# Kernel optimization log

Measured on AMD Instinct MI355X. Metric: run time of the kernel, lower is better.

Reference implementation:

```python
import jax, jax.numpy as jnp
import numpy as np

DILATIONS = (1, 2, 4, 8, 16, 32, 64, 128, 256, 512)
K = 3            # kernel_size
CH = 128         # channels
B, T = 4, 16384
L = len(DILATIONS)


def _conv1x1(x, w, b=None):
    # x: [B, Cin, T], w: [Cout, Cin, 1] -> [B, Cout, T]
    y = jnp.einsum('oc,bct->bot', w[..., 0], x)
    return y if b is None else y + b[None, :, None]


def _causal_dilated_conv(x, w, b, d):
    # buffer of zeros of size (K-1)*d concatenated on the left == causal left pad
    pad = (K - 1) * d
    y = jax.lax.conv_general_dilated(
        x, w, window_strides=(1,), padding=[(pad, 0)], rhs_dilation=(d,),
        dimension_numbers=('NCH', 'OIH', 'NCH'))
    return y + b[None, :, None]


def setup_inputs() -> dict:
    key = jax.random.key(0)
    ks = jax.random.split(key, 12)
    s = 0.1  # keep gated activations out of saturation
    return {
        'x': jax.random.normal(ks[0], (B, 1, T), jnp.float32),
        'c': jax.random.normal(ks[1], (B, 1, T), jnp.float32),
        'head_init': jnp.zeros((B, CH, T), jnp.float32),
        'w_re': jax.random.normal(ks[2], (CH, 1, 1), jnp.float32) * s,
        'conv_w': jax.random.normal(ks[3], (L, 2 * CH, CH, K), jnp.float32) * s,
        'conv_b': jax.random.normal(ks[4], (L, 2 * CH), jnp.float32) * s,
        'mix_w': jax.random.normal(ks[5], (L, 2 * CH, 1, 1), jnp.float32) * s,
        'w1x1': jax.random.normal(ks[6], (L, CH, CH, 1), jnp.float32) * s,
        'b1x1': jax.random.normal(ks[7], (L, CH), jnp.float32) * s,
        'w_head': jax.random.normal(ks[8], (1, CH, 1), jnp.float32) * s,
        'b_head': jax.random.normal(ks[9], (1,), jnp.float32) * s,
    }


def reference(x, c, head_init, w_re, conv_w, conv_b, mix_w, w1x1, b1x1, w_head, b_head):
    h = _conv1x1(x, w_re)               # rechannel: [B, CH, T]
    head = head_init                    # head accumulator (zeros == head_input=None)
    for li, d in enumerate(DILATIONS):  # fixed small layer loop (structurally distinct dilations)
        z = _causal_dilated_conv(h, conv_w[li], conv_b[li], d)   # [B, 2CH, T]
        z = z + _conv1x1(c, mix_w[li])                           # conditioning mixer
        post = jnp.tanh(z[:, :CH]) * jax.nn.sigmoid(z[:, CH:])   # gated activation
        h = h + _conv1x1(post, w1x1[li], b1x1[li])               # residual
        head = head + post
    out = _conv1x1(head, w_head, b_head)  # [B, 1, T]
    return out, h
```

## Files before the change

kernel.cpp:

```cpp
#include <hip/hip_runtime.h>
#include <hip/hip_bf16.h>

#define B_   4
#define T_   16384
#define CH_  128
#define TCH_ 256
#define NL_  10
#define TT_  64
#define SHW_ 196

typedef __attribute__((ext_vector_type(8))) short short8;
typedef __attribute__((ext_vector_type(16))) float f32x16;

#define MFMA32(a, b, c) __builtin_amdgcn_mfma_f32_32x32x16_bf16(a, b, c, 0, 0, 0)

__device__ __forceinline__ unsigned short f2bf(float f) {
  unsigned u = __float_as_uint(f);
  return (unsigned short)((u + 0x7FFFu + ((u >> 16) & 1u)) >> 16);
}
__device__ __forceinline__ unsigned pk2bf(float lo, float hi) {
  unsigned r;
  asm("v_cvt_pk_bf16_f32 %0, %1, %2" : "=v"(r) : "v"(lo), "v"(hi));
  return r;
}
__device__ __forceinline__ float bf2f(unsigned s) {
  return __uint_as_float((s & 0xFFFFu) << 16);
}
__device__ __forceinline__ float fast_tanh(float x) {
  float e = __expf(2.0f * fabsf(x));
  float t = 1.0f - 2.0f / (e + 1.0f);
  return copysignf(t, x);
}
__device__ __forceinline__ float fast_sig(float x) {
  return 1.0f / (1.0f + __expf(-x));
}

__global__ __launch_bounds__(256) void pack_w(
    const float* __restrict__ conv_w, const float* __restrict__ w1x1,
    unsigned short* __restrict__ wpackA, unsigned short* __restrict__ wpack1) {
  const int NA = NL_ * 8 * 24 * 64 * 8;
  int idx = blockIdx.x * 256 + threadIdx.x;
  if (idx < NA) {
    int j = idx & 7;
    int l = (idx >> 3) & 63;
    int t2 = idx >> 9;
    int ks = t2 % 24;
    int t3 = t2 / 24;
    int of = t3 & 7;
    int li = t3 >> 3;
    int o = 32 * of + (l & 31);
    int ck = 16 * ks + 8 * (l >> 5) + j;
    int c = ck & 127, ktap = ck >> 7;
    wpackA[idx] = f2bf(conv_w[((li * TCH_ + o) * CH_ + c) * 3 + ktap]);
  } else {
    int i2 = idx - NA;
    if (i2 < NL_ * 4 * 8 * 64 * 8) {
      int j = i2 & 7;
      int l = (i2 >> 3) & 63;
      int ks = (i2 >> 9) & 7;
      int of = (i2 >> 12) & 3;
      int li = i2 >> 14;
      int o = 32 * of + (l & 31);
      int c = 16 * ks + 8 * (l >> 5) + j;
      wpack1[i2] = f2bf(w1x1[(li * CH_ + o) * CH_ + c]);
    }
  }
}

__global__ __launch_bounds__(256) void rechannel_k(
    const float* __restrict__ x, const float* __restrict__ w_re,
    unsigned short* __restrict__ hb) {
  int flat = blockIdx.x * 256 + threadIdx.x;
  int cid = flat & 15;
  int t = (flat >> 4) & (T_ - 1);
  int b = flat >> 18;
  float xv = x[b * T_ + t];
  const float* wr = w_re + cid * 8;
  union { short8 s; unsigned short u[8]; } o;
#pragma unroll
  for (int j = 0; j < 8; ++j) o.u[j] = f2bf(wr[j] * xv);
  *(short8*)(hb + (size_t)(b * T_ + t) * CH_ + cid * 8) = o.s;
}

__global__ __launch_bounds__(256) void out_init_k(
    const float* __restrict__ head_init, const float* __restrict__ w_head,
    const float* __restrict__ b_head, float* __restrict__ out) {
  int idx = blockIdx.x * 256 + threadIdx.x;
  int b = idx / T_;
  int t = idx - b * T_;
  float acc = b_head[0];
#pragma unroll 8
  for (int c = 0; c < CH_; ++c)
    acc += w_head[c] * head_init[(b * CH_ + c) * T_ + t];
  out[idx] = acc;
}

__global__ __launch_bounds__(256, 3) void layer_k(
    const unsigned short* __restrict__ hin,
    unsigned short* __restrict__ hob,
    float* __restrict__ hof,
    const float* __restrict__ cin, float* __restrict__ out,
    const unsigned short* __restrict__ wA,
    const unsigned short* __restrict__ w1p,
    const float* __restrict__ bconv,
    const float* __restrict__ wmix,
    const float* __restrict__ b1,
    const float* __restrict__ w_head,
    int d, int is_final) {
  __shared__ unsigned shH[TT_ * SHW_];
  __shared__ float shR[4 * 64];

  const int tid = threadIdx.x;
  const int b = blockIdx.y;
  const int tile = (blockIdx.x & 7) * 32 + (blockIdx.x >> 3);
  const int t0 = tile * TT_;

#pragma unroll
  for (int it = 0; it < 12; ++it) {
    int flat = it * 256 + tid;
    int cid = flat & 15;
    int tt = (flat >> 4) & 63;
    int k = flat >> 10;
    int t = t0 + tt - (2 - k) * d;
    uint4 v = make_uint4(0u, 0u, 0u, 0u);
    if (t >= 0)
      v = *(const uint4*)(hin + ((size_t)(b * T_ + t) * CH_ + cid * 8));
    *(uint4*)(shH + tt * SHW_ + k * 64 + cid * 4) = v;
  }
  __syncthreads();

  const int wave = __builtin_amdgcn_readfirstlane(tid >> 6);
  const int lane = tid & 63;
  const int ln = lane & 31;
  const int kg = lane >> 5;

  f32x16 aL0, aL1, aH0, aH1;
#pragma unroll
  for (int i = 0; i < 16; ++i) { aL0[i] = 0.f; aL1[i] = 0.f; aH0[i] = 0.f; aH1[i] = 0.f; }

  const short8* wAv = (const short8*)wA;
#pragma unroll
  for (int ks = 0; ks < 24; ++ks) {
    short8 b0 = *(const short8*)(shH + ln * SHW_ + 8 * ks + 4 * kg);
    short8 b1f = *(const short8*)(shH + (32 + ln) * SHW_ + 8 * ks + 4 * kg);
    short8 alo = wAv[(wave * 24 + ks) * 64 + lane];
    short8 ahi = wAv[((wave + 4) * 24 + ks) * 64 + lane];
    aL0 = MFMA32(alo, b0, aL0);
    aL1 = MFMA32(alo, b1f, aL1);
    aH0 = MFMA32(ahi, b0, aH0);
    aH1 = MFMA32(ahi, b1f, aH1);
  }
  __syncthreads();

  const float cq0 = cin[b * T_ + t0 + ln];
  const float cq1 = cin[b * T_ + t0 + 32 + ln];
  float hs0 = 0.f, hs1 = 0.f;
#pragma unroll
  for (int r2 = 0; r2 < 4; ++r2) {
    const int o4 = 32 * wave + 8 * r2 + 4 * kg;
    const float4 bcL = *(const float4*)(bconv + o4);
    const float4 bcH = *(const float4*)(bconv + CH_ + o4);
    const float4 wmL = *(const float4*)(wmix + o4);
    const float4 wmH = *(const float4*)(wmix + CH_ + o4);
    const float4 wh = *(const float4*)(w_head + o4);
    float pv0[4], pv1[4];
#pragma unroll
    for (int j2 = 0; j2 < 4; ++j2) {
      const float bl = ((const float*)&bcL)[j2], bh = ((const float*)&bcH)[j2];
      const float ml = ((const float*)&wmL)[j2], mh = ((const float*)&wmH)[j2];
      const float w = ((const float*)&wh)[j2];
      float zl0 = aL0[4 * r2 + j2] + bl + ml * cq0;
      float zh0 = aH0[4 * r2 + j2] + bh + mh * cq0;
      pv0[j2] = fast_tanh(zl0) * fast_sig(zh0);
      hs0 += w * pv0[j2];
      float zl1 = aL1[4 * r2 + j2] + bl + ml * cq1;
      float zh1 = aH1[4 * r2 + j2] + bh + mh * cq1;
      pv1[j2] = fast_tanh(zl1) * fast_sig(zh1);
      hs1 += w * pv1[j2];
    }
    uint2 pk;
    const int dw = 16 * wave + 4 * r2 + 2 * kg;
    pk.x = pk2bf(pv0[0], pv0[1]);
    pk.y = pk2bf(pv0[2], pv0[3]);
    *(uint2*)(shH + ln * SHW_ + dw) = pk;
    pk.x = pk2bf(pv1[0], pv1[1]);
    pk.y = pk2bf(pv1[2], pv1[3]);
    *(uint2*)(shH + (32 + ln) * SHW_ + dw) = pk;
  }
  hs0 += __shfl_xor(hs0, 32);
  hs1 += __shfl_xor(hs1, 32);
  if (lane < 32) {
    shR[wave * 64 + ln] = hs0;
    shR[wave * 64 + 32 + ln] = hs1;
  }
  __syncthreads();

  f32x16 d0, d1;
#pragma unroll
  for (int i = 0; i < 16; ++i) { d0[i] = 0.f; d1[i] = 0.f; }

  const short8* w1v = (const short8*)w1p;
#pragma unroll
  for (int ks = 0; ks < 8; ++ks) {
    short8 p0 = *(const short8*)(shH + ln * SHW_ + 8 * ks + 4 * kg);
    short8 p1 = *(const short8*)(shH + (32 + ln) * SHW_ + 8 * ks + 4 * kg);
    short8 a = w1v[(wave * 8 + ks) * 64 + lane];
    d0 = MFMA32(a, p0, d0);
    d1 = MFMA32(a, p1, d1);
  }

  if (tid < 64) {
    float tot = shR[tid] + shR[64 + tid] + shR[128 + tid] + shR[192 + tid];
    out[b * T_ + t0 + tid] += tot;
  }

  float res0[16], res1[16];
#pragma unroll
  for (int r2 = 0; r2 < 4; ++r2) {
    const int o4 = 32 * wave + 8 * r2 + 4 * kg;
    const float4 b14 = *(const float4*)(b1 + o4);
    const int dw = 16 * wave + 4 * r2 + 2 * kg;
    uint2 h0 = *(const uint2*)(shH + ln * SHW_ + 128 + dw);
    uint2 h1 = *(const uint2*)(shH + (32 + ln) * SHW_ + 128 + dw);
    res0[4 * r2 + 0] = bf2f(h0.x) + ((const float*)&b14)[0] + d0[4 * r2 + 0];
    res0[4 * r2 + 1] = bf2f(h0.x >> 16) + ((const float*)&b14)[1] + d0[4 * r2 + 1];
    res0[4 * r2 + 2] = bf2f(h0.y) + ((const float*)&b14)[2] + d0[4 * r2 + 2];
    res0[4 * r2 + 3] = bf2f(h0.y >> 16) + ((const float*)&b14)[3] + d0[4 * r2 + 3];
    res1[4 * r2 + 0] = bf2f(h1.x) + ((const float*)&b14)[0] + d1[4 * r2 + 0];
    res1[4 * r2 + 1] = bf2f(h1.x >> 16) + ((const float*)&b14)[1] + d1[4 * r2 + 1];
    res1[4 * r2 + 2] = bf2f(h1.y) + ((const float*)&b14)[2] + d1[4 * r2 + 2];
    res1[4 * r2 + 3] = bf2f(h1.y >> 16) + ((const float*)&b14)[3] + d1[4 * r2 + 3];
  }

  if (!is_final) {
    __syncthreads();
#pragma unroll
    for (int r2 = 0; r2 < 4; ++r2) {
      const int dw = 16 * wave + 4 * r2 + 2 * kg;
      uint2 pk;
      pk.x = pk2bf(res0[4 * r2 + 0], res0[4 * r2 + 1]);
      pk.y = pk2bf(res0[4 * r2 + 2], res0[4 * r2 + 3]);
      *(uint2*)(shH + ln * SHW_ + dw) = pk;
      pk.x = pk2bf(res1[4 * r2 + 0], res1[4 * r2 + 1]);
      pk.y = pk2bf(res1[4 * r2 + 2], res1[4 * r2 + 3]);
      *(uint2*)(shH + (32 + ln) * SHW_ + dw) = pk;
    }
    __syncthreads();
#pragma unroll
    for (int it = 0; it < 4; ++it) {
      int flat = it * 256 + tid;
      int cid = flat & 15;
      int tt = flat >> 4;
      *(uint4*)(hob + ((size_t)(b * T_ + t0 + tt) * CH_ + cid * 8)) =
          *(const uint4*)(shH + tt * SHW_ + cid * 4);
    }
  } else {
#pragma unroll
    for (int r2 = 0; r2 < 4; ++r2) {
#pragma unroll
      for (int j2 = 0; j2 < 4; ++j2) {
        const int o = 32 * wave + 8 * r2 + 4 * kg + j2;
        hof[(size_t)(b * CH_ + o) * T_ + t0 + ln] = res0[4 * r2 + j2];
        hof[(size_t)(b * CH_ + o) * T_ + t0 + 32 + ln] = res1[4 * r2 + j2];
      }
    }
  }
}

extern "C" void kernel_launch(void* const* d_in, const int* in_sizes, int n_in,
                              void* d_out, int out_size, void* d_ws, size_t ws_size,
                              hipStream_t stream) {
  const float* x         = (const float*)d_in[0];
  const float* c         = (const float*)d_in[1];
  const float* head_init = (const float*)d_in[2];
  const float* w_re      = (const float*)d_in[3];
  const float* conv_w    = (const float*)d_in[4];
  const float* conv_b    = (const float*)d_in[5];
  const float* mix_w     = (const float*)d_in[6];
  const float* w1x1      = (const float*)d_in[7];
  const float* b1x1      = (const float*)d_in[8];
  const float* w_head    = (const float*)d_in[9];
  const float* b_head    = (const float*)d_in[10];

  float* out = (float*)d_out;
  float* hof = out + B_ * T_;

  unsigned short* hb0 = (unsigned short*)d_ws;
  unsigned short* hb1 = hb0 + (size_t)B_ * T_ * CH_;
  unsigned short* wpackA = hb1 + (size_t)B_ * T_ * CH_;
  unsigned short* wpack1 = wpackA + NL_ * 8 * 24 * 64 * 8;

  const int n_pack = NL_ * 8 * 24 * 64 * 8 + NL_ * 4 * 8 * 64 * 8;
  pack_w<<<(n_pack + 255) / 256, 256, 0, stream>>>(conv_w, w1x1, wpackA, wpack1);

  rechannel_k<<<(B_ * T_ * 16) / 256, 256, 0, stream>>>(x, w_re, hb0);
  out_init_k<<<(B_ * T_) / 256, 256, 0, stream>>>(head_init, w_head, b_head, out);

  const int dil[NL_] = {1, 2, 4, 8, 16, 32, 64, 128, 256, 512};
  for (int li = 0; li < NL_; ++li) {
    const unsigned short* hin = (li & 1) ? hb1 : hb0;
    unsigned short* hob       = (li & 1) ? hb0 : hb1;
    int is_final = (li == NL_ - 1);
    layer_k<<<dim3(T_ / TT_, B_), 256, 0, stream>>>(
        hin, hob, hof, c, out,
        wpackA + li * (8 * 24 * 64 * 8),
        wpack1 + li * (4 * 8 * 64 * 8),
        conv_b + li * TCH_,
        mix_w + li * TCH_,
        b1x1 + li * CH_,
        w_head,
        dil[li], is_final);
  }
}
```

Baseline: 310.8 us.

## Share overlapping dilated-conv tap windows in LDS and raise occupancy

```diff
diff --git a/kernel.cpp b/kernel.cpp
--- a/kernel.cpp
+++ b/kernel.cpp
@@ -7,7 +7,7 @@
 #define TCH_ 256
 #define NL_  10
 #define TT_  64
-#define SHW_ 196
+#define SWW_ 68
 
 typedef __attribute__((ext_vector_type(8))) short short8;
 typedef __attribute__((ext_vector_type(16))) float f32x16;
@@ -95,7 +95,7 @@
   out[idx] = acc;
 }
 
-__global__ __launch_bounds__(256, 3) void layer_k(
+__global__ __launch_bounds__(256, 4) void layer_k(
     const unsigned short* __restrict__ hin,
     unsigned short* __restrict__ hob,
     float* __restrict__ hof,
@@ -107,7 +107,7 @@
     const float* __restrict__ b1,
     const float* __restrict__ w_head,
     int d, int is_final) {
-  __shared__ unsigned shH[TT_ * SHW_];
+  __shared__ unsigned shW[128 * SWW_];
   __shared__ float shR[4 * 64];
 
   const int tid = threadIdx.x;
@@ -115,17 +115,19 @@
   const int tile = (blockIdx.x & 7) * 32 + (blockIdx.x >> 3);
   const int t0 = tile * TT_;
 
-#pragma unroll
-  for (int it = 0; it < 12; ++it) {
-    int flat = it * 256 + tid;
+  const bool smallD = (d <= 32);
+  const int NW = smallD ? 64 + 2 * d : 128;
+
+  for (int flat = tid; flat < NW * 16; flat += 256) {
     int cid = flat & 15;
-    int tt = (flat >> 4) & 63;
-    int k = flat >> 10;
-    int t = t0 + tt - (2 - k) * d;
+    int rw = flat >> 4;
+    int t;
+    if (smallD) t = t0 - 2 * d + rw;
+    else        t = (rw < 64) ? (t0 - 2 * d + rw) : (t0 - d + (rw - 64));
     uint4 v = make_uint4(0u, 0u, 0u, 0u);
     if (t >= 0)
       v = *(const uint4*)(hin + ((size_t)(b * T_ + t) * CH_ + cid * 8));
-    *(uint4*)(shH + tt * SHW_ + k * 64 + cid * 4) = v;
+    *(uint4*)(shW + rw * SWW_ + cid * 4) = v;
   }
   __syncthreads();
 
@@ -139,16 +141,62 @@
   for (int i = 0; i < 16; ++i) { aL0[i] = 0.f; aL1[i] = 0.f; aH0[i] = 0.f; aH1[i] = 0.f; }
 
   const short8* wAv = (const short8*)wA;
-#pragma unroll
-  for (int ks = 0; ks < 24; ++ks) {
-    short8 b0 = *(const short8*)(shH + ln * SHW_ + 8 * ks + 4 * kg);
-    short8 b1f = *(const short8*)(shH + (32 + ln) * SHW_ + 8 * ks + 4 * kg);
-    short8 alo = wAv[(wave * 24 + ks) * 64 + lane];
-    short8 ahi = wAv[((wave + 4) * 24 + ks) * 64 + lane];
-    aL0 = MFMA32(alo, b0, aL0);
-    aL1 = MFMA32(alo, b1f, aL1);
-    aH0 = MFMA32(ahi, b0, aH0);
-    aH1 = MFMA32(ahi, b1f, aH1);
+  if (smallD) {
+#pragma unroll
+    for (int ks = 0; ks < 24; ++ks) {
+      const int k = ks >> 3, cb = ks & 7;
+      const int r0 = ln + k * d;
+      short8 b0 = *(const short8*)(shW + r0 * SWW_ + 8 * cb + 4 * kg);
+      short8 b1f = *(const short8*)(shW + (r0 + 32) * SWW_ + 8 * cb + 4 * kg);
+      short8 alo = wAv[(wave * 24 + ks) * 64 + lane];
+      short8 ahi = wAv[((wave + 4) * 24 + ks) * 64 + lane];
+      aL0 = MFMA32(alo, b0, aL0);
+      aL1 = MFMA32(alo, b1f, aL1);
+      aH0 = MFMA32(ahi, b0, aH0);
+      aH1 = MFMA32(ahi, b1f, aH1);
+    }
+  } else {
+#pragma unroll
+    for (int ks = 0; ks < 16; ++ks) {
+      const int k = ks >> 3, cb = ks & 7;
+      const int r0 = 64 * k + ln;
+      short8 b0 = *(const short8*)(shW + r0 * SWW_ + 8 * cb + 4 * kg);
+      short8 b1f = *(const short8*)(shW + (r0 + 32) * SWW_ + 8 * cb + 4 * kg);
+      short8 alo = wAv[(wave * 24 + ks) * 64 + lane];
+      short8 ahi = wAv[((wave + 4) * 24 + ks) * 64 + lane];
+      aL0 = MFMA32(alo, b0, aL0);
+      aL1 = MFMA32(alo, b1f, aL1);
+      aH0 = MFMA32(ahi, b0, aH0);
+      aH1 = MFMA32(ahi, b1f, aH1);
+    }
+    const unsigned short* hrow0 = hin + (size_t)(b * T_ + t0 + ln) * CH_;
+    const unsigned short* hrow1 = hrow0 + (size_t)32 * CH_;
+#pragma unroll
+    for (int cb = 0; cb < 8; ++cb) {
+      short8 b0 = *(const short8*)(hrow0 + 16 * cb + 8 * kg);
+      short8 b1f = *(const short8*)(hrow1 + 16 * cb + 8 * kg);
+      short8 alo = wAv[(wave * 24 + 16 + cb) * 64 + lane];
+      short8 ahi = wAv[((wave + 4) * 24 + 16 + cb) * 64 + lane];
+      aL0 = MFMA32(alo, b0, aL0);
+      aL1 = MFMA32(alo, b1f, aL1);
+      aH0 = MFMA32(ahi, b0, aH0);
+      aH1 = MFMA32(ahi, b1f, aH1);
+    }
+  }
+  __syncthreads();
+
+  uint2 ct0[4], ct1[4];
+#pragma unroll
+  for (int r2 = 0; r2 < 4; ++r2) {
+    const int dw = 16 * wave + 4 * r2 + 2 * kg;
+    if (smallD) {
+      ct0[r2] = *(const uint2*)(shW + (2 * d + ln) * SWW_ + dw);
+      ct1[r2] = *(const uint2*)(shW + (2 * d + 32 + ln) * SWW_ + dw);
+    } else {
+      const int o4 = 2 * dw;
+      ct0[r2] = *(const uint2*)(hin + (size_t)(b * T_ + t0 + ln) * CH_ + o4);
+      ct1[r2] = *(const uint2*)(hin + (size_t)(b * T_ + t0 + 32 + ln) * CH_ + o4);
+    }
   }
   __syncthreads();
 
@@ -182,10 +230,10 @@
     const int dw = 16 * wave + 4 * r2 + 2 * kg;
     pk.x = pk2bf(pv0[0], pv0[1]);
     pk.y = pk2bf(pv0[2], pv0[3]);
-    *(uint2*)(shH + ln * SHW_ + dw) = pk;
+    *(uint2*)(shW + ln * SWW_ + dw) = pk;
     pk.x = pk2bf(pv1[0], pv1[1]);
     pk.y = pk2bf(pv1[2], pv1[3]);
-    *(uint2*)(shH + (32 + ln) * SHW_ + dw) = pk;
+    *(uint2*)(shW + (32 + ln) * SWW_ + dw) = pk;
   }
   hs0 += __shfl_xor(hs0, 32);
   hs1 += __shfl_xor(hs1, 32);
@@ -202,8 +250,8 @@
   const short8* w1v = (const short8*)w1p;
 #pragma unroll
   for (int ks = 0; ks < 8; ++ks) {
-    short8 p0 = *(const short8*)(shH + ln * SHW_ + 8 * ks + 4 * kg);
-    short8 p1 = *(const short8*)(shH + (32 + ln) * SHW_ + 8 * ks + 4 * kg);
+    short8 p0 = *(const short8*)(shW + ln * SWW_ + 8 * ks + 4 * kg);
+    short8 p1 = *(const short8*)(shW + (32 + ln) * SWW_ + 8 * ks + 4 * kg);
     short8 a = w1v[(wave * 8 + ks) * 64 + lane];
     d0 = MFMA32(a, p0, d0);
     d1 = MFMA32(a, p1, d1);
@@ -219,17 +267,14 @@
   for (int r2 = 0; r2 < 4; ++r2) {
     const int o4 = 32 * wave + 8 * r2 + 4 * kg;
     const float4 b14 = *(const float4*)(b1 + o4);
-    const int dw = 16 * wave + 4 * r2 + 2 * kg;
-    uint2 h0 = *(const uint2*)(shH + ln * SHW_ + 128 + dw);
-    uint2 h1 = *(const uint2*)(shH + (32 + ln) * SHW_ + 128 + dw);
-    res0[4 * r2 + 0] = bf2f(h0.x) + ((const float*)&b14)[0] + d0[4 * r2 + 0];
-    res0[4 * r2 + 1] = bf2f(h0.x >> 16) + ((const float*)&b14)[1] + d0[4 * r2 + 1];
-    res0[4 * r2 + 2] = bf2f(h0.y) + ((const float*)&b14)[2] + d0[4 * r2 + 2];
-    res0[4 * r2 + 3] = bf2f(h0.y >> 16) + ((const float*)&b14)[3] + d0[4 * r2 + 3];
-    res1[4 * r2 + 0] = bf2f(h1.x) + ((const float*)&b14)[0] + d1[4 * r2 + 0];
-    res1[4 * r2 + 1] = bf2f(h1.x >> 16) + ((const float*)&b14)[1] + d1[4 * r2 + 1];
-    res1[4 * r2 + 2] = bf2f(h1.y) + ((const float*)&b14)[2] + d1[4 * r2 + 2];
-    res1[4 * r2 + 3] = bf2f(h1.y >> 16) + ((const float*)&b14)[3] + d1[4 * r2 + 3];
+    res0[4 * r2 + 0] = bf2f(ct0[r2].x) + ((const float*)&b14)[0] + d0[4 * r2 + 0];
+    res0[4 * r2 + 1] = bf2f(ct0[r2].x >> 16) + ((const float*)&b14)[1] + d0[4 * r2 + 1];
+    res0[4 * r2 + 2] = bf2f(ct0[r2].y) + ((const float*)&b14)[2] + d0[4 * r2 + 2];
+    res0[4 * r2 + 3] = bf2f(ct0[r2].y >> 16) + ((const float*)&b14)[3] + d0[4 * r2 + 3];
+    res1[4 * r2 + 0] = bf2f(ct1[r2].x) + ((const float*)&b14)[0] + d1[4 * r2 + 0];
+    res1[4 * r2 + 1] = bf2f(ct1[r2].x >> 16) + ((const float*)&b14)[1] + d1[4 * r2 + 1];
+    res1[4 * r2 + 2] = bf2f(ct1[r2].y) + ((const float*)&b14)[2] + d1[4 * r2 + 2];
+    res1[4 * r2 + 3] = bf2f(ct1[r2].y >> 16) + ((const float*)&b14)[3] + d1[4 * r2 + 3];
   }
 
   if (!is_final) {
@@ -240,10 +285,10 @@
       uint2 pk;
       pk.x = pk2bf(res0[4 * r2 + 0], res0[4 * r2 + 1]);
       pk.y = pk2bf(res0[4 * r2 + 2], res0[4 * r2 + 3]);
-      *(uint2*)(shH + ln * SHW_ + dw) = pk;
+      *(uint2*)(shW + ln * SWW_ + dw) = pk;
       pk.x = pk2bf(res1[4 * r2 + 0], res1[4 * r2 + 1]);
       pk.y = pk2bf(res1[4 * r2 + 2], res1[4 * r2 + 3]);
-      *(uint2*)(shH + (32 + ln) * SHW_ + dw) = pk;
+      *(uint2*)(shW + (32 + ln) * SWW_ + dw) = pk;
     }
     __syncthreads();
 #pragma unroll
@@ -252,7 +297,7 @@
       int cid = flat & 15;
       int tt = flat >> 4;
       *(uint4*)(hob + ((size_t)(b * T_ + t0 + tt) * CH_ + cid * 8)) =
-          *(const uint4*)(shH + tt * SHW_ + cid * 4);
+          *(const uint4*)(shW + tt * SWW_ + cid * 4);
     }
   } else {
 #pragma unroll
```

Result: slower. 542.8 us (+74.6%).
